# Kernel optimization log

Hardware: AMD Instinct MI355X
Metric: run time of the kernel (lower is better)

## Reference

```python
import jax, jax.numpy as jnp
import numpy as np

MAXV = 127.0  # 2**(8-1) - 1, signed int8


def setup_inputs() -> dict:
    key = jax.random.key(0)
    k1, k2, k3 = jax.random.split(key, 3)
    N, K, M = 8192, 4096, 4096  # tokens, size_in, size_out
    x = jax.random.normal(k1, (N, K), dtype=jnp.float32)
    weight = jax.random.normal(k2, (M, K), dtype=jnp.float32) * 0.02
    bias = jax.random.normal(k3, (M,), dtype=jnp.float32) * 0.01
    amax_x = jnp.array([3.0], dtype=jnp.float32)   # calibrated activation amax
    amax_w = jnp.array([0.06], dtype=jnp.float32)  # calibrated weight amax
    return {"x": x, "weight": weight, "bias": bias, "amax_x": amax_x, "amax_w": amax_w}


def _quantize_int8(v, amax):
    # TensorQuantizer with fake_quant=False: scale to int grid, round, clamp to [-127, 127]
    return jnp.clip(jnp.round(v * (MAXV / amax)), -MAXV, MAXV).astype(jnp.int8)


def reference(x, weight, bias, amax_x, amax_w):
    qx = _quantize_int8(x, amax_x)          # [N, K] int8
    qw = _quantize_int8(weight, amax_w)     # [M, K] int8
    acc = jnp.matmul(qx.astype(jnp.int32), qw.T.astype(jnp.int32))  # [N, M] int32
    scale = (MAXV / amax_x) * (MAXV / amax_w)  # combined dequant scale
    out = acc.astype(jnp.float32) / scale
    return out + bias
```

## Files before the change

kernel.cpp:

```cpp
#include <hip/hip_runtime.h>

typedef __attribute__((ext_vector_type(4))) int i32x4;

__device__ __forceinline__ void gload_lds16(const void* g, void* l) {
  __builtin_amdgcn_global_load_lds((const __attribute__((address_space(1))) void*)g,
                                   (__attribute__((address_space(3))) void*)l,
                                   16, 0, 0);
}

__device__ __forceinline__ int swz4(int r) { return (r ^ (r >> 2)) & 3; }

__global__ void quant_i8_kernel(const float* __restrict__ in,
                                signed char* __restrict__ out,
                                const float* __restrict__ amax, int n4) {
  const float s = 127.0f / amax[0];
  int i = blockIdx.x * blockDim.x + threadIdx.x;
  const int stride = gridDim.x * blockDim.x;
  const float4* __restrict__ in4 = (const float4*)in;
  int* __restrict__ o4 = (int*)out;
  for (; i < n4; i += stride) {
    float4 v = in4[i];
    int q0 = (int)rintf(fminf(fmaxf(v.x * s, -127.0f), 127.0f));
    int q1 = (int)rintf(fminf(fmaxf(v.y * s, -127.0f), 127.0f));
    int q2 = (int)rintf(fminf(fmaxf(v.z * s, -127.0f), 127.0f));
    int q3 = (int)rintf(fminf(fmaxf(v.w * s, -127.0f), 127.0f));
    o4[i] = (q0 & 255) | ((q1 & 255) << 8) | ((q2 & 255) << 16) | ((q3 & 255) << 24);
  }
}

__global__ __launch_bounds__(256, 2) void gemm_i8_kernel(
    const signed char* __restrict__ qx,
    const signed char* __restrict__ qw,
    const float* __restrict__ bias,
    const float* __restrict__ amax_x,
    const float* __restrict__ amax_w,
    float* __restrict__ out,
    int N, int M, int K) {
  constexpr int BM = 128;
  constexpr int BN = 128;
  constexpr int BK = 64;

  __shared__ alignas(16) signed char As[BM * BK];
  __shared__ alignas(16) signed char Bs[BN * BK];

  const int tid  = threadIdx.x;
  const int wid  = tid >> 6;
  const int lane = tid & 63;
  const int l15  = lane & 15;
  const int l4   = lane >> 4;

  const int rowBase = blockIdx.y * BM;
  const int colBase = blockIdx.x * BN;

  const int wRow = (wid >> 1) * 64;
  const int wCol = (wid & 1) * 64;

  const int tr = tid >> 2;
  const int tp = tid & 3;
  const int ra = tr, rb = tr + 64;
  const int ca0 = (tp ^ swz4(ra)) * 16;
  const int ca1 = (tp ^ swz4(rb)) * 16;

  const signed char* srcA0 = qx + (size_t)(rowBase + ra) * K + ca0;
  const signed char* srcA1 = qx + (size_t)(rowBase + rb) * K + ca1;
  const signed char* srcB0 = qw + (size_t)(colBase + ra) * K + ca0;
  const signed char* srcB1 = qw + (size_t)(colBase + rb) * K + ca1;

  i32x4 acc[4][4] = {};

  int offA[4], offB[4];
#pragma unroll
  for (int i = 0; i < 4; ++i) {
    int r = wRow + i * 16 + l15;
    offA[i] = r * 64 + (l4 ^ swz4(r)) * 16;
    int c = wCol + i * 16 + l15;
    offB[i] = c * 64 + (l4 ^ swz4(c)) * 16;
  }

  for (int kt = 0; kt < K; kt += BK) {
    gload_lds16(srcA0 + kt, As + tid * 16);
    gload_lds16(srcA1 + kt, As + 4096 + tid * 16);
    gload_lds16(srcB0 + kt, Bs + tid * 16);
    gload_lds16(srcB1 + kt, Bs + 4096 + tid * 16);
    __syncthreads();

    i32x4 a[4], b[4];
#pragma unroll
    for (int i = 0; i < 4; ++i) a[i] = *(const i32x4*)(As + offA[i]);
#pragma unroll
    for (int j = 0; j < 4; ++j) b[j] = *(const i32x4*)(Bs + offB[j]);

#pragma unroll
    for (int i = 0; i < 4; ++i)
#pragma unroll
      for (int j = 0; j < 4; ++j)
        acc[i][j] = __builtin_amdgcn_mfma_i32_16x16x64_i8(a[i], b[j], acc[i][j], 0, 0, 0);

    __syncthreads();
  }

  const float dq = amax_x[0] * amax_w[0] * (1.0f / (127.0f * 127.0f));
#pragma unroll
  for (int j = 0; j < 4; ++j) {
    const int col = colBase + wCol + j * 16 + l15;
    const float bv = bias[col];
#pragma unroll
    for (int i = 0; i < 4; ++i) {
      const int row = rowBase + wRow + i * 16 + l4 * 4;
#pragma unroll
      for (int r = 0; r < 4; ++r) {
        out[(size_t)(row + r) * M + col] = (float)acc[i][j][r] * dq + bv;
      }
    }
  }
}

extern "C" void kernel_launch(void* const* d_in, const int* in_sizes, int n_in,
                              void* d_out, int out_size, void* d_ws, size_t ws_size,
                              hipStream_t stream) {
  const float* x      = (const float*)d_in[0];
  const float* w      = (const float*)d_in[1];
  const float* bias   = (const float*)d_in[2];
  const float* amax_x = (const float*)d_in[3];
  const float* amax_w = (const float*)d_in[4];
  float* out = (float*)d_out;

  const int M = in_sizes[2];
  const int K = in_sizes[1] / M;
  const int N = (int)((long)in_sizes[0] / K);

  signed char* qx = (signed char*)d_ws;
  signed char* qw = qx + (size_t)N * K;

  quant_i8_kernel<<<2048, 256, 0, stream>>>(x, qx, amax_x, N * (K / 4));
  quant_i8_kernel<<<2048, 256, 0, stream>>>(w, qw, amax_w, M * (K / 4));

  dim3 grid(M / 128, N / 128);
  gemm_i8_kernel<<<grid, 256, 0, stream>>>(qx, qw, bias, amax_x, amax_w, out,
                                           N, M, K);
}
```

Measured before the change: 220.4 us.

## Rewrite int8 GEMM as 256x256 tile, 8-wave ping-pong pipelined kernel

Replaces the 128x128 single-buffered int8 MFMA GEMM with a 256x256 tile, 512-thread kernel. It uses double-buffered LDS with K=128 steps, interleaves global-to-LDS staging with MFMA quadrants under explicit barriers and waitcnts, and raises MFMA priority with setprio. Block IDs are remapped so neighbouring blocks share input tiles in cache, and an XOR swizzle avoids LDS bank conflicts. The aim is to hide memory latency and raise data reuse per block. The cost is 128KB of LDS per block, which limits occupancy, plus a fragile hand-tuned schedule.

```diff
diff --git a/kernel.cpp b/kernel.cpp
--- a/kernel.cpp
+++ b/kernel.cpp
@@ -8,7 +8,9 @@
                                    16, 0, 0);
 }
 
-__device__ __forceinline__ int swz4(int r) { return (r ^ (r >> 2)) & 3; }
+#define BARRIER() __builtin_amdgcn_s_barrier()
+#define LGKM0()   asm volatile("s_waitcnt lgkmcnt(0)" ::: "memory")
+#define VMCNT4()  asm volatile("s_waitcnt vmcnt(4)" ::: "memory")
 
 __global__ void quant_i8_kernel(const float* __restrict__ in,
                                 signed char* __restrict__ out,
@@ -28,7 +30,7 @@
   }
 }
 
-__global__ __launch_bounds__(256, 2) void gemm_i8_kernel(
+__global__ __launch_bounds__(512, 2) void gemm_i8_8p(
     const signed char* __restrict__ qx,
     const signed char* __restrict__ qw,
     const float* __restrict__ bias,
@@ -36,83 +38,160 @@
     const float* __restrict__ amax_w,
     float* __restrict__ out,
     int N, int M, int K) {
-  constexpr int BM = 128;
-  constexpr int BN = 128;
-  constexpr int BK = 64;
-
-  __shared__ alignas(16) signed char As[BM * BK];
-  __shared__ alignas(16) signed char Bs[BN * BK];
+  constexpr int BKB = 128;
+
+  __shared__ signed char lds[4][256 * 128];
 
   const int tid  = threadIdx.x;
+  const int lane = tid & 63;
   const int wid  = tid >> 6;
-  const int lane = tid & 63;
+  const int wm   = wid >> 2;
+  const int wn   = wid & 3;
   const int l15  = lane & 15;
   const int l4   = lane >> 4;
 
-  const int rowBase = blockIdx.y * BM;
-  const int colBase = blockIdx.x * BN;
-
-  const int wRow = (wid >> 1) * 64;
-  const int wCol = (wid & 1) * 64;
-
-  const int tr = tid >> 2;
-  const int tp = tid & 3;
-  const int ra = tr, rb = tr + 64;
-  const int ca0 = (tp ^ swz4(ra)) * 16;
-  const int ca1 = (tp ^ swz4(rb)) * 16;
-
-  const signed char* srcA0 = qx + (size_t)(rowBase + ra) * K + ca0;
-  const signed char* srcA1 = qx + (size_t)(rowBase + rb) * K + ca1;
-  const signed char* srcB0 = qw + (size_t)(colBase + ra) * K + ca0;
-  const signed char* srcB1 = qw + (size_t)(colBase + rb) * K + ca1;
-
-  i32x4 acc[4][4] = {};
-
-  int offA[4], offB[4];
-#pragma unroll
-  for (int i = 0; i < 4; ++i) {
-    int r = wRow + i * 16 + l15;
-    offA[i] = r * 64 + (l4 ^ swz4(r)) * 16;
-    int c = wCol + i * 16 + l15;
-    offB[i] = c * 64 + (l4 ^ swz4(c)) * 16;
-  }
-
-  for (int kt = 0; kt < K; kt += BK) {
-    gload_lds16(srcA0 + kt, As + tid * 16);
-    gload_lds16(srcA1 + kt, As + 4096 + tid * 16);
-    gload_lds16(srcB0 + kt, Bs + tid * 16);
-    gload_lds16(srcB1 + kt, Bs + 4096 + tid * 16);
-    __syncthreads();
-
-    i32x4 a[4], b[4];
-#pragma unroll
-    for (int i = 0; i < 4; ++i) a[i] = *(const i32x4*)(As + offA[i]);
-#pragma unroll
-    for (int j = 0; j < 4; ++j) b[j] = *(const i32x4*)(Bs + offB[j]);
-
-#pragma unroll
-    for (int i = 0; i < 4; ++i)
-#pragma unroll
-      for (int j = 0; j < 4; ++j)
-        acc[i][j] = __builtin_amdgcn_mfma_i32_16x16x64_i8(a[i], b[j], acc[i][j], 0, 0, 0);
-
-    __syncthreads();
+  const int nbn = M >> 8;
+  const int nwg = (N >> 8) * nbn;
+  const int cpx = nwg >> 3;
+  const int swz = (blockIdx.x & 7) * cpx + (blockIdx.x >> 3);
+  const int rowBase = (swz / nbn) << 8;
+  const int colBase = (swz % nbn) << 8;
+
+  const signed char* sA[2][2];
+  const signed char* sB[2][2];
+#pragma unroll
+  for (int h = 0; h < 2; ++h)
+#pragma unroll
+    for (int L = 0; L < 2; ++L) {
+      const int slot = h * 1024 + L * 512 + tid;
+      const int row  = slot >> 3;
+      const int c    = (slot & 7) ^ (row & 7);
+      sA[h][L] = qx + (size_t)(rowBase + row) * K + c * 16;
+      sB[h][L] = qw + (size_t)(colBase + row) * K + c * 16;
+    }
+
+  signed char* A0 = lds[0];
+  signed char* B0 = lds[1];
+  signed char* A1 = lds[2];
+  signed char* B1 = lds[3];
+
+#define STAGE(dst, src, h, kt)                                             \
+  do {                                                                     \
+    gload_lds16(src[h][0] + (kt) * BKB, (dst) + (h)*16384 + tid * 16);     \
+    gload_lds16(src[h][1] + (kt) * BKB, (dst) + (h)*16384 + 8192 + tid * 16); \
+  } while (0)
+
+  const int ck0 = ((l4) ^ (l15 & 7)) * 16;
+  const int ck1 = ((4 + l4) ^ (l15 & 7)) * 16;
+  const int aRow0 = (wm * 128 + l15) * 128;
+  const int bRow0 = (wn * 64 + l15) * 128;
+
+  i32x4 acc[8][4] = {{{0}}};
+  i32x4 af[4][2];
+  i32x4 bf[4][2];
+
+#define RDA(R, mb)                                                          \
+  {                                                                         \
+    _Pragma("unroll") for (int mi = 0; mi < 4; ++mi) {                      \
+      af[mi][0] = *(const i32x4*)((R) + aRow0 + ((mb) + mi) * 2048 + ck0);  \
+      af[mi][1] = *(const i32x4*)((R) + aRow0 + ((mb) + mi) * 2048 + ck1);  \
+    }                                                                       \
+  }
+#define RDB(R, nb)                                                          \
+  {                                                                         \
+    _Pragma("unroll") for (int nj = 0; nj < 2; ++nj) {                      \
+      bf[(nb) + nj][0] = *(const i32x4*)((R) + bRow0 + ((nb) + nj) * 2048 + ck0); \
+      bf[(nb) + nj][1] = *(const i32x4*)((R) + bRow0 + ((nb) + nj) * 2048 + ck1); \
+    }                                                                       \
+  }
+#define MFMAQ(mb, nb)                                                       \
+  {                                                                         \
+    _Pragma("unroll") for (int mi = 0; mi < 4; ++mi)                        \
+        _Pragma("unroll") for (int nj = 0; nj < 2; ++nj)                    \
+            _Pragma("unroll") for (int ks = 0; ks < 2; ++ks)                \
+                acc[(mb) + mi][(nb) + nj] = __builtin_amdgcn_mfma_i32_16x16x64_i8( \
+                    af[mi][ks], bf[(nb) + nj][ks], acc[(mb) + mi][(nb) + nj], 0, 0, 0); \
+  }
+
+  const int T = K / BKB;
+
+  STAGE(B0, sB, 0, 0); STAGE(B0, sB, 1, 0);
+  STAGE(A0, sA, 0, 0); STAGE(A0, sA, 1, 0);
+  STAGE(B1, sB, 0, 1); STAGE(B1, sB, 1, 1);
+  VMCNT4();
+  BARRIER();
+
+  for (int it = 0; it < T / 2; ++it) {
+    const int k1 = 2 * it + 1;
+    const int k2 = (2 * it + 2 < T) ? 2 * it + 2 : T - 1;
+    const int k3 = (2 * it + 3 < T) ? 2 * it + 3 : T - 1;
+
+    RDA(A0, 0); RDB(B0, 0);
+    STAGE(A1, sA, 0, k1);
+    BARRIER(); LGKM0();
+    __builtin_amdgcn_s_setprio(1); MFMAQ(0, 0); __builtin_amdgcn_s_setprio(0);
+    BARRIER();
+
+    RDB(B0, 2);
+    STAGE(A1, sA, 1, k1);
+    BARRIER(); LGKM0();
+    __builtin_amdgcn_s_setprio(1); MFMAQ(0, 2); __builtin_amdgcn_s_setprio(0);
+    BARRIER();
+
+    RDA(A0, 4);
+    STAGE(B0, sB, 0, k2);
+    BARRIER(); LGKM0();
+    __builtin_amdgcn_s_setprio(1); MFMAQ(4, 0); __builtin_amdgcn_s_setprio(0);
+    BARRIER();
+
+    STAGE(B0, sB, 1, k2);
+    BARRIER(); LGKM0();
+    __builtin_amdgcn_s_setprio(1); MFMAQ(4, 2); __builtin_amdgcn_s_setprio(0);
+    VMCNT4();
+    BARRIER();
+
+    RDA(A1, 0); RDB(B1, 0);
+    STAGE(A0, sA, 0, k2);
+    BARRIER(); LGKM0();
+    __builtin_amdgcn_s_setprio(1); MFMAQ(0, 0); __builtin_amdgcn_s_setprio(0);
+    BARRIER();
+
+    RDB(B1, 2);
+    STAGE(A0, sA, 1, k2);
+    BARRIER(); LGKM0();
+    __builtin_amdgcn_s_setprio(1); MFMAQ(0, 2); __builtin_amdgcn_s_setprio(0);
+    BARRIER();
+
+    RDA(A1, 4);
+    STAGE(B1, sB, 0, k3);
+    BARRIER(); LGKM0();
+    __builtin_amdgcn_s_setprio(1); MFMAQ(4, 0); __builtin_amdgcn_s_setprio(0);
+    BARRIER();
+
+    STAGE(B1, sB, 1, k3);
+    BARRIER(); LGKM0();
+    __builtin_amdgcn_s_setprio(1); MFMAQ(4, 2); __builtin_amdgcn_s_setprio(0);
+    VMCNT4();
+    BARRIER();
   }
 
   const float dq = amax_x[0] * amax_w[0] * (1.0f / (127.0f * 127.0f));
 #pragma unroll
-  for (int j = 0; j < 4; ++j) {
-    const int col = colBase + wCol + j * 16 + l15;
+  for (int nj = 0; nj < 4; ++nj) {
+    const int col = colBase + wn * 64 + nj * 16 + l15;
     const float bv = bias[col];
 #pragma unroll
-    for (int i = 0; i < 4; ++i) {
-      const int row = rowBase + wRow + i * 16 + l4 * 4;
-#pragma unroll
-      for (int r = 0; r < 4; ++r) {
-        out[(size_t)(row + r) * M + col] = (float)acc[i][j][r] * dq + bv;
-      }
+    for (int mi = 0; mi < 8; ++mi) {
+      const int row = rowBase + wm * 128 + mi * 16 + l4 * 4;
+#pragma unroll
+      for (int r = 0; r < 4; ++r)
+        out[(size_t)(row + r) * M + col] = (float)acc[mi][nj][r] * dq + bv;
     }
   }
+#undef STAGE
+#undef RDA
+#undef RDB
+#undef MFMAQ
 }
 
 extern "C" void kernel_launch(void* const* d_in, const int* in_sizes, int n_in,
@@ -135,7 +214,7 @@
   quant_i8_kernel<<<2048, 256, 0, stream>>>(x, qx, amax_x, N * (K / 4));
   quant_i8_kernel<<<2048, 256, 0, stream>>>(w, qw, amax_w, M * (K / 4));
 
-  dim3 grid(M / 128, N / 128);
-  gemm_i8_kernel<<<grid, 256, 0, stream>>>(qx, qw, bias, amax_x, amax_w, out,
-                                           N, M, K);
-}
+  const int nwg = (N / 256) * (M / 256);
+  gemm_i8_8p<<<nwg, 512, 0, stream>>>(qx, qw, bias, amax_x, amax_w, out,
+                                      N, M, K);
+}
```

Measured after the change: 191.8 us. -13.0%, faster.
